# Performance work log

Hardware: AMD Instinct MI355X
Metric: run time of the kernel (lower is better)

Reference implementation:

```python
import jax, jax.numpy as jnp
import numpy as np

H = 51  # hidden size hard-coded in the module

def lstm_cell(x, h, c, W_ih, W_hh, b_ih, b_hh):
    # PyTorch LSTMCell: gates = x @ W_ih^T + b_ih + h @ W_hh^T + b_hh
    g = x @ W_ih.T + h @ W_hh.T + (b_ih + b_hh)  # [B, 4H]
    i, f, gg, o = jnp.split(g, 4, axis=-1)
    c_new = jax.nn.sigmoid(f) * c + jax.nn.sigmoid(i) * jnp.tanh(gg)
    h_new = jax.nn.sigmoid(o) * jnp.tanh(c_new)
    return h_new, c_new

def setup_inputs() -> dict:
    key = jax.random.key(0)
    ks = jax.random.split(key, 12)
    B, T = 2048, 2048
    s1 = 1.0 / np.sqrt(H)
    u = lambda k, shape: jax.random.uniform(k, shape, jnp.float32, -s1, s1)
    return {
        "input": jax.random.normal(ks[0], (B, T), jnp.float32),
        "W_ih1": u(ks[1], (4 * H, 1)),
        "W_hh1": u(ks[2], (4 * H, H)),
        "b_ih1": u(ks[3], (4 * H,)),
        "b_hh1": u(ks[4], (4 * H,)),
        "W_ih2": u(ks[5], (4 * H, H)),
        "W_hh2": u(ks[6], (4 * H, H)),
        "b_ih2": u(ks[7], (4 * H,)),
        "b_hh2": u(ks[8], (4 * H,)),
        "W_lin": u(ks[9], (1, H)),
        "b_lin": u(ks[10], (1,)),
    }

def reference(input, W_ih1, W_hh1, b_ih1, b_hh1, W_ih2, W_hh2, b_ih2, b_hh2, W_lin, b_lin):
    B, T = input.shape
    xs = input.T[:, :, None]  # [T, B, 1]
    h1 = jnp.zeros((B, H), input.dtype)
    c1 = jnp.zeros((B, H), input.dtype)
    h2 = jnp.zeros((B, H), input.dtype)
    c2 = jnp.zeros((B, H), input.dtype)

    def step(carry, x_t):
        h1, c1, h2, c2 = carry
        h1, c1 = lstm_cell(x_t, h1, c1, W_ih1, W_hh1, b_ih1, b_hh1)
        h2, c2 = lstm_cell(h1, h2, c2, W_ih2, W_hh2, b_ih2, b_hh2)
        y = h2 @ W_lin.T + b_lin  # [B, 1]
        return (h1, c1, h2, c2), y[:, 0]

    _, ys = jax.lax.scan(step, (h1, c1, h2, c2), xs)  # ys: [T, B]
    return ys.T  # [B, T]
```

## Files before the change

### kernel.cpp

```cpp
#include <hip/hip_runtime.h>

#define H 51
#define TSEQ 2048
#define BB 16
#define THREADS 1024

typedef _Float16 __attribute__((ext_vector_type(8))) half8;
typedef float    __attribute__((ext_vector_type(4))) float4v;

#define LOG2E    1.44269504f
#define TWOLOG2E 2.88539008f

__device__ __forceinline__ float lstm_ew(float4v a, float& c) {
    float eA = __builtin_amdgcn_exp2f(-a[0]);
    float eB = __builtin_amdgcn_exp2f(a[2]);
    float eF = __builtin_amdgcn_exp2f(-a[1]);
    float pA = eA + 1.0f, pB = eB + 1.0f, pF = eF + 1.0f;
    float dAB = pA * pB;
    float t0  = fmaf(eB, pF, -pF);
    float num = fmaf(c, dAB, t0);
    float r   = __builtin_amdgcn_rcpf(dAB * pF);
    float cn  = num * r;
    c = cn;
    float uD = fminf(cn * TWOLOG2E, 126.0f);
    float eD = __builtin_amdgcn_exp2f(uD);
    float eC = __builtin_amdgcn_exp2f(-a[3]);
    float pD = eD + 1.0f;
    float r2 = __builtin_amdgcn_rcpf(fmaf(eC, pD, pD));
    return fmaf(eD, r2, -r2);
}

__global__ __launch_bounds__(THREADS)
void lstm_w16h_kernel(const float* __restrict__ input,
                      const float* __restrict__ W_ih1, const float* __restrict__ W_hh1,
                      const float* __restrict__ b_ih1, const float* __restrict__ b_hh1,
                      const float* __restrict__ W_ih2, const float* __restrict__ W_hh2,
                      const float* __restrict__ b_ih2, const float* __restrict__ b_hh2,
                      const float* __restrict__ W_lin, const float* __restrict__ b_lin,
                      float* __restrict__ out)
{
    __shared__ half8 hb1[2][2][64];
    __shared__ half8 hb2[2][2][64];
    __shared__ float xss[2][64 * 17];
    __shared__ float ybf[128][17];

    const int tid  = threadIdx.x;
    const int wv   = tid >> 6;
    const int lane = tid & 63;
    const int n    = lane & 15;
    const int qd   = lane >> 4;
    const int b0   = blockIdx.x * BB;
    const float blin = b_lin[0];

    if (tid < 256) {
        half8 z = {0,0,0,0,0,0,0,0};
        (&hb1[0][0][0])[tid] = z;
        (&hb2[0][0][0])[tid] = z;
    }

    if (wv == 15) {
#pragma unroll
        for (int k = 0; k < 16; ++k)
            xss[0][lane * 17 + k] = input[(size_t)(b0 + k) * TSEQ + lane];
    }

    half8 wa1[2];
    half8 wa2[4];
    {
        const int tw1 = (wv < 12) ? wv : ((wv == 13) ? 12 : 13);
        const int tw2 = (wv < 12) ? wv : ((wv == 14) ? 12 : 13);
        {
            const int arow = tw1 * 16 + n;
            const int cell = arow >> 2, gate = arow & 3;
            const int orow = gate * H + cell;
            const float gsc = (gate == 2) ? TWOLOG2E : LOG2E;
            const bool rok = (arow < 4 * H);
#pragma unroll
            for (int s = 0; s < 2; ++s)
#pragma unroll
                for (int j = 0; j < 8; ++j) {
                    int kk = s * 32 + qd * 8 + j;
                    float w = 0.f;
                    if (rok) {
                        if (kk < H)        w = gsc * W_hh1[orow * H + kk];
                        else if (kk == 51) w = gsc * W_ih1[orow];
                    }
                    wa1[s][j] = (_Float16)w;
                }
        }
        {
            const int arow = tw2 * 16 + n;
            const int cell = arow >> 2, gate = arow & 3;
            const int orow = gate * H + cell;
            const float gsc = (gate == 2) ? TWOLOG2E : LOG2E;
            const bool rok = (arow < 4 * H);
#pragma unroll
            for (int s = 0; s < 4; ++s)
#pragma unroll
                for (int j = 0; j < 8; ++j) {
                    int kk = s * 32 + qd * 8 + j;
                    float w = 0.f;
                    if (rok) {
                        if (kk < H)                       w = gsc * W_ih2[orow * H + kk];
                        else if (kk >= 64 && kk < 64 + H) w = gsc * W_hh2[orow * H + (kk - 64)];
                    } else if (arow == 204) {
                        if (kk >= 64 && kk < 64 + H)      w = W_lin[kk - 64];
                    }
                    wa2[s][j] = (_Float16)w;
                }
        }
    }

    const int ewv = (wv == 13 || wv == 14) ? 12 : ((wv < 12) ? wv : 13);
    const int jj  = ewv * 4 + qd;
    float4v bias1v, wih1v, bias2v;
    {
        const bool cok1 = (jj < H) && (wv < 12 || wv == 13);
        const bool cok2 = (jj < H) && (wv < 12 || wv == 14);
#pragma unroll
        for (int r = 0; r < 4; ++r) {
            const float gsc = (r == 2) ? TWOLOG2E : LOG2E;
            const int orow = r * H + jj;
            bias1v[r] = cok1 ? gsc * (b_ih1[orow] + b_hh1[orow]) : 0.f;
            wih1v[r]  = cok1 ? gsc * W_ih1[orow] : 0.f;
            bias2v[r] = cok2 ? gsc * (b_ih2[orow] + b_hh2[orow]) : 0.f;
        }
    }

    float c1 = 0.f, c2 = 0.f;
    const int js = jj >> 5, jq = (jj & 31) >> 3, j7 = jj & 7;

    __syncthreads();

    if (wv < 12 || wv == 13) {
        const float xb = xss[0][n];
        float4v a;
#pragma unroll
        for (int r = 0; r < 4; ++r) a[r] = fmaf(wih1v[r], xb, bias1v[r]);
        float h = lstm_ew(a, c1);
        if (!(wv == 13 && qd == 3))
            ((_Float16*)&hb1[0][js][jq * 16 + n])[j7] = (_Float16)h;
    } else if (wv == 15) {
        if (lane < 16)
            ((_Float16*)&hb1[0][1][32 + lane])[3] = (_Float16)xss[0][17 + lane];
    }
    __syncthreads();

#define STEP(t, P)                                                              \
    {                                                                           \
        if (wv < 12) {                                                          \
               \
            half8 g1[2], g2[2];                                                 \
            g1[0] = hb1[P][0][lane];      g1[1] = hb1[P][1][lane];              \
            float4v a1 = bias1v;                                                \
            a1 = __builtin_amdgcn_mfma_f32_16x16x32_f16(wa1[0], g1[0], a1, 0, 0, 0); \
            a1 = __builtin_amdgcn_mfma_f32_16x16x32_f16(wa1[1], g1[1], a1, 0, 0, 0); \
            float4v a2 = bias2v;                                                \
            a2 = __builtin_amdgcn_mfma_f32_16x16x32_f16(wa2[0], g1[0], a2, 0, 0, 0); \
            a2 = __builtin_amdgcn_mfma_f32_16x16x32_f16(wa2[1], g1[1], a2, 0, 0, 0); \
            __builtin_amdgcn_sched_barrier(0);                                  \
                   \
            g2[0] = hb2[P ^ 1][0][lane];  g2[1] = hb2[P ^ 1][1][lane];          \
            {                                                                   \
                float h = lstm_ew(a1, c1);                                      \
                ((_Float16*)&hb1[P ^ 1][js][jq * 16 + n])[j7] = (_Float16)h;    \
            }                                                                   \
            a2 = __builtin_amdgcn_mfma_f32_16x16x32_f16(wa2[2], g2[0], a2, 0, 0, 0); \
            a2 = __builtin_amdgcn_mfma_f32_16x16x32_f16(wa2[3], g2[1], a2, 0, 0, 0); \
            {                                                                   \
                float h = lstm_ew(a2, c2);                                      \
                ((_Float16*)&hb2[P][js][jq * 16 + n])[j7] = (_Float16)h;        \
            }                                                                   \
        } else if (wv == 12) {                                                  \
               \
            if ((t) > 64 && ((t) & 63) == 1) {                                  \
                const int tb = (t) - 65;                                        \
                const int sb = tb & 127;                                        \
                _Pragma("unroll")                                               \
                for (int r = 0; r < BB; ++r)                                    \
                    out[(size_t)(b0 + r) * TSEQ + tb + lane] = ybf[sb + lane][r]; \
            }                                                                   \
        } else if (wv == 13) {                                                  \
                     \
            half8 g1[2];                                                        \
            g1[0] = hb1[P][0][lane];      g1[1] = hb1[P][1][lane];              \
            float4v a1 = bias1v;                                                \
            a1 = __builtin_amdgcn_mfma_f32_16x16x32_f16(wa1[0], g1[0], a1, 0, 0, 0); \
            a1 = __builtin_amdgcn_mfma_f32_16x16x32_f16(wa1[1], g1[1], a1, 0, 0, 0); \
            float h = lstm_ew(a1, c1);                                          \
            if (qd != 3)                                                        \
                ((_Float16*)&hb1[P ^ 1][js][jq * 16 + n])[j7] = (_Float16)h;    \
        } else if (wv == 14) {                                                  \
               \
            half8 g1[2], g2[2];                                                 \
            g1[0] = hb1[P][0][lane];      g1[1] = hb1[P][1][lane];              \
            float4v a2 = bias2v;                                                \
            a2 = __builtin_amdgcn_mfma_f32_16x16x32_f16(wa2[0], g1[0], a2, 0, 0, 0); \
            a2 = __builtin_amdgcn_mfma_f32_16x16x32_f16(wa2[1], g1[1], a2, 0, 0, 0); \
            __builtin_amdgcn_sched_barrier(0);                                  \
            g2[0] = hb2[P ^ 1][0][lane];  g2[1] = hb2[P ^ 1][1][lane];          \
            a2 = __builtin_amdgcn_mfma_f32_16x16x32_f16(wa2[2], g2[0], a2, 0, 0, 0); \
            a2 = __builtin_amdgcn_mfma_f32_16x16x32_f16(wa2[3], g2[1], a2, 0, 0, 0); \
            float h = lstm_ew(a2, c2);                                          \
            ((_Float16*)&hb2[P][js][jq * 16 + n])[j7] = (_Float16)h;            \
            if (qd == 3) ybf[((t) - 1) & 127][n] = a2[0] + blin;    \
        } else {                                                                \
                \
            const int t2 = (t) + 2;                                             \
            if (lane < 16) {                                                    \
                float xf = xss[(t2 >> 6) & 1][(t2 & 63) * 17 + lane];           \
                ((_Float16*)&hb1[P ^ 1][1][32 + lane])[3] = (_Float16)xf;       \
            }                                                                   \
            if (((t) & 63) == 32 && (t) + 32 < TSEQ) {                          \
                const int cp = ((t) >> 6) & 1;                                  \
                _Pragma("unroll")                                               \
                for (int k = 0; k < 16; ++k)                                    \
                    xss[cp ^ 1][lane * 17 + k] =                                \
                        input[(size_t)(b0 + k) * TSEQ + ((t) + 32) + lane];     \
            }                                                                   \
        }                                                                       \
        __syncthreads();                                                        \
    }

#pragma unroll 1
    for (int t = 0; t < TSEQ; t += 2) {
        STEP(t, 0)
        STEP(t + 1, 1)
    }
#undef STEP

    if (wv == 14) {
        half8 g2a = hb2[1][0][lane], g2b = hb2[1][1][lane];
        float4v yb = (float4v){0.f, 0.f, 0.f, 0.f};
        yb = __builtin_amdgcn_mfma_f32_16x16x32_f16(wa2[2], g2a, yb, 0, 0, 0);
        yb = __builtin_amdgcn_mfma_f32_16x16x32_f16(wa2[3], g2b, yb, 0, 0, 0);
        if (qd == 3) ybf[127][n] = yb[0] + blin;
    }
    __syncthreads();
    if (wv == 12) {
        const int tb = TSEQ - 64;
#pragma unroll
        for (int r = 0; r < BB; ++r)
            out[(size_t)(b0 + r) * TSEQ + tb + lane] = ybf[64 + lane][r];
    }
}

extern "C" void kernel_launch(void* const* d_in, const int* in_sizes, int n_in,
                              void* d_out, int out_size, void* d_ws, size_t ws_size,
                              hipStream_t stream) {
    const float* input = (const float*)d_in[0];
    const float* W_ih1 = (const float*)d_in[1];
    const float* W_hh1 = (const float*)d_in[2];
    const float* b_ih1 = (const float*)d_in[3];
    const float* b_hh1 = (const float*)d_in[4];
    const float* W_ih2 = (const float*)d_in[5];
    const float* W_hh2 = (const float*)d_in[6];
    const float* b_ih2 = (const float*)d_in[7];
    const float* b_hh2 = (const float*)d_in[8];
    const float* W_lin = (const float*)d_in[9];
    const float* b_lin = (const float*)d_in[10];

    lstm_w16h_kernel<<<dim3(2048 / BB), dim3(THREADS), 0, stream>>>(
        input, W_ih1, W_hh1, b_ih1, b_hh1,
        W_ih2, W_hh2, b_ih2, b_hh2, W_lin, b_lin,
        (float*)d_out);
}
```

Measured before the change: 1.209 ms.

## Process two 16-row batch groups per block to interleave independent recurrences

Doubles the batch rows per block to 32, split into two independent 16-row groups. Each wave runs both groups' MFMA and gate chains between the same barriers. This is meant to hide MFMA and transcendental latency through instruction-level parallelism and to amortise per-step barrier cost. In exchange the grid halves to 64 blocks, leaving more CUs idle, and each block does twice the serial work per step.

Result: slower. 1.977 ms (+63.6%).

```diff
diff --git a/kernel.cpp b/kernel.cpp
--- a/kernel.cpp
+++ b/kernel.cpp
@@ -2,7 +2,7 @@
 
 #define H 51
 #define TSEQ 2048
-#define BB 16
+#define BB 32
 #define THREADS 1024
 
 typedef _Float16 __attribute__((ext_vector_type(8))) half8;
@@ -31,18 +31,18 @@
 }
 
 __global__ __launch_bounds__(THREADS)
-void lstm_w16h_kernel(const float* __restrict__ input,
-                      const float* __restrict__ W_ih1, const float* __restrict__ W_hh1,
-                      const float* __restrict__ b_ih1, const float* __restrict__ b_hh1,
-                      const float* __restrict__ W_ih2, const float* __restrict__ W_hh2,
-                      const float* __restrict__ b_ih2, const float* __restrict__ b_hh2,
-                      const float* __restrict__ W_lin, const float* __restrict__ b_lin,
-                      float* __restrict__ out)
+void lstm_w32_kernel(const float* __restrict__ input,
+                     const float* __restrict__ W_ih1, const float* __restrict__ W_hh1,
+                     const float* __restrict__ b_ih1, const float* __restrict__ b_hh1,
+                     const float* __restrict__ W_ih2, const float* __restrict__ W_hh2,
+                     const float* __restrict__ b_ih2, const float* __restrict__ b_hh2,
+                     const float* __restrict__ W_lin, const float* __restrict__ b_lin,
+                     float* __restrict__ out)
 {
-    __shared__ half8 hb1[2][2][64];
-    __shared__ half8 hb2[2][2][64];
-    __shared__ float xss[2][64 * 17];
-    __shared__ float ybf[128][17];
+    __shared__ half8 hb1[2][2][2][64];
+    __shared__ half8 hb2[2][2][2][64];
+    __shared__ float xss[2][2][64 * 17];
+    __shared__ float ybf[2][128][17];
 
     const int tid  = threadIdx.x;
     const int wv   = tid >> 6;
@@ -52,16 +52,17 @@
     const int b0   = blockIdx.x * BB;
     const float blin = b_lin[0];
 
-    if (tid < 256) {
+    if (tid < 512) {
         half8 z = {0,0,0,0,0,0,0,0};
-        (&hb1[0][0][0])[tid] = z;
-        (&hb2[0][0][0])[tid] = z;
+        (&hb1[0][0][0][0])[tid] = z;
+        (&hb2[0][0][0][0])[tid] = z;
     }
 
     if (wv == 15) {
 #pragma unroll
-        for (int k = 0; k < 16; ++k)
-            xss[0][lane * 17 + k] = input[(size_t)(b0 + k) * TSEQ + lane];
+        for (int k = 0; k < 32; ++k)
+            xss[k >> 4][0][lane * 17 + (k & 15)] =
+                input[(size_t)(b0 + k) * TSEQ + lane];
     }
 
     half8 wa1[2];
@@ -127,95 +128,143 @@
         }
     }
 
-    float c1 = 0.f, c2 = 0.f;
+    float c1A = 0.f, c2A = 0.f, c1B = 0.f, c2B = 0.f;
     const int js = jj >> 5, jq = (jj & 31) >> 3, j7 = jj & 7;
 
     __syncthreads();
 
     if (wv < 12 || wv == 13) {
-        const float xb = xss[0][n];
-        float4v a;
-#pragma unroll
-        for (int r = 0; r < 4; ++r) a[r] = fmaf(wih1v[r], xb, bias1v[r]);
-        float h = lstm_ew(a, c1);
-        if (!(wv == 13 && qd == 3))
-            ((_Float16*)&hb1[0][js][jq * 16 + n])[j7] = (_Float16)h;
+        const float xbA = xss[0][0][n];
+        const float xbB = xss[1][0][n];
+        float4v aA, aB;
+#pragma unroll
+        for (int r = 0; r < 4; ++r) {
+            aA[r] = fmaf(wih1v[r], xbA, bias1v[r]);
+            aB[r] = fmaf(wih1v[r], xbB, bias1v[r]);
+        }
+        float hA = lstm_ew(aA, c1A);
+        float hB = lstm_ew(aB, c1B);
+        if (!(wv == 13 && qd == 3)) {
+            ((_Float16*)&hb1[0][0][js][jq * 16 + n])[j7] = (_Float16)hA;
+            ((_Float16*)&hb1[1][0][js][jq * 16 + n])[j7] = (_Float16)hB;
+        }
     } else if (wv == 15) {
-        if (lane < 16)
-            ((_Float16*)&hb1[0][1][32 + lane])[3] = (_Float16)xss[0][17 + lane];
+        if (lane < 32) {
+            int g = lane >> 4, nn = lane & 15;
+            ((_Float16*)&hb1[g][0][1][32 + nn])[3] = (_Float16)xss[g][0][17 + nn];
+        }
     }
     __syncthreads();
 
 #define STEP(t, P)                                                              \
     {                                                                           \
         if (wv < 12) {                                                          \
-               \
-            half8 g1[2], g2[2];                                                 \
-            g1[0] = hb1[P][0][lane];      g1[1] = hb1[P][1][lane];              \
-            float4v a1 = bias1v;                                                \
-            a1 = __builtin_amdgcn_mfma_f32_16x16x32_f16(wa1[0], g1[0], a1, 0, 0, 0); \
-            a1 = __builtin_amdgcn_mfma_f32_16x16x32_f16(wa1[1], g1[1], a1, 0, 0, 0); \
-            float4v a2 = bias2v;                                                \
-            a2 = __builtin_amdgcn_mfma_f32_16x16x32_f16(wa2[0], g1[0], a2, 0, 0, 0); \
-            a2 = __builtin_amdgcn_mfma_f32_16x16x32_f16(wa2[1], g1[1], a2, 0, 0, 0); \
+              \
+            half8 g1A[2], g1B[2], g2A[2], g2B[2];                               \
+            g1A[0] = hb1[0][P][0][lane];  g1A[1] = hb1[0][P][1][lane];          \
+            g1B[0] = hb1[1][P][0][lane];  g1B[1] = hb1[1][P][1][lane];          \
+            float4v a1A = bias1v;                                               \
+            a1A = __builtin_amdgcn_mfma_f32_16x16x32_f16(wa1[0], g1A[0], a1A, 0, 0, 0); \
+            a1A = __builtin_amdgcn_mfma_f32_16x16x32_f16(wa1[1], g1A[1], a1A, 0, 0, 0); \
+            float4v a1B = bias1v;                                               \
+            a1B = __builtin_amdgcn_mfma_f32_16x16x32_f16(wa1[0], g1B[0], a1B, 0, 0, 0); \
+            a1B = __builtin_amdgcn_mfma_f32_16x16x32_f16(wa1[1], g1B[1], a1B, 0, 0, 0); \
+            float4v a2A = bias2v;                                               \
+            a2A = __builtin_amdgcn_mfma_f32_16x16x32_f16(wa2[0], g1A[0], a2A, 0, 0, 0); \
+            a2A = __builtin_amdgcn_mfma_f32_16x16x32_f16(wa2[1], g1A[1], a2A, 0, 0, 0); \
+            float4v a2B = bias2v;                                               \
+            a2B = __builtin_amdgcn_mfma_f32_16x16x32_f16(wa2[0], g1B[0], a2B, 0, 0, 0); \
+            a2B = __builtin_amdgcn_mfma_f32_16x16x32_f16(wa2[1], g1B[1], a2B, 0, 0, 0); \
             __builtin_amdgcn_sched_barrier(0);                                  \
-                   \
-            g2[0] = hb2[P ^ 1][0][lane];  g2[1] = hb2[P ^ 1][1][lane];          \
+              \
+            g2A[0] = hb2[0][P ^ 1][0][lane];  g2A[1] = hb2[0][P ^ 1][1][lane];  \
+            g2B[0] = hb2[1][P ^ 1][0][lane];  g2B[1] = hb2[1][P ^ 1][1][lane];  \
             {                                                                   \
-                float h = lstm_ew(a1, c1);                                      \
-                ((_Float16*)&hb1[P ^ 1][js][jq * 16 + n])[j7] = (_Float16)h;    \
-            }                                                                   \
-            a2 = __builtin_amdgcn_mfma_f32_16x16x32_f16(wa2[2], g2[0], a2, 0, 0, 0); \
-            a2 = __builtin_amdgcn_mfma_f32_16x16x32_f16(wa2[3], g2[1], a2, 0, 0, 0); \
+                float h = lstm_ew(a1A, c1A);                                    \
+                ((_Float16*)&hb1[0][P ^ 1][js][jq * 16 + n])[j7] = (_Float16)h; \
+            }                                                                   \
             {                                                                   \
-                float h = lstm_ew(a2, c2);                                      \
-                ((_Float16*)&hb2[P][js][jq * 16 + n])[j7] = (_Float16)h;        \
+                float h = lstm_ew(a1B, c1B);                                    \
+                ((_Float16*)&hb1[1][P ^ 1][js][jq * 16 + n])[j7] = (_Float16)h; \
+            }                                                                   \
+            a2A = __builtin_amdgcn_mfma_f32_16x16x32_f16(wa2[2], g2A[0], a2A, 0, 0, 0); \
+            a2A = __builtin_amdgcn_mfma_f32_16x16x32_f16(wa2[3], g2A[1], a2A, 0, 0, 0); \
+            a2B = __builtin_amdgcn_mfma_f32_16x16x32_f16(wa2[2], g2B[0], a2B, 0, 0, 0); \
+            a2B = __builtin_amdgcn_mfma_f32_16x16x32_f16(wa2[3], g2B[1], a2B, 0, 0, 0); \
+            {                                                                   \
+                float h = lstm_ew(a2A, c2A);                                    \
+                ((_Float16*)&hb2[0][P][js][jq * 16 + n])[j7] = (_Float16)h;     \
+            }                                                                   \
+            {                                                                   \
+                float h = lstm_ew(a2B, c2B);                                    \
+                ((_Float16*)&hb2[1][P][js][jq * 16 + n])[j7] = (_Float16)h;     \
             }                                                                   \
         } else if (wv == 12) {                                                  \
-               \
+                \
             if ((t) > 64 && ((t) & 63) == 1) {                                  \
                 const int tb = (t) - 65;                                        \
                 const int sb = tb & 127;                                        \
                 _Pragma("unroll")                                               \
                 for (int r = 0; r < BB; ++r)                                    \
-                    out[(size_t)(b0 + r) * TSEQ + tb + lane] = ybf[sb + lane][r]; \
+                    out[(size_t)(b0 + r) * TSEQ + tb + lane] =                  \
+                        ybf[r >> 4][sb + lane][r & 15];                         \
             }                                                                   \
         } else if (wv == 13) {                                                  \
-                     \
-            half8 g1[2];                                                        \
-            g1[0] = hb1[P][0][lane];      g1[1] = hb1[P][1][lane];              \
-            float4v a1 = bias1v;                                                \
-            a1 = __builtin_amdgcn_mfma_f32_16x16x32_f16(wa1[0], g1[0], a1, 0, 0, 0); \
-            a1 = __builtin_amdgcn_mfma_f32_16x16x32_f16(wa1[1], g1[1], a1, 0, 0, 0); \
-            float h = lstm_ew(a1, c1);                                          \
-            if (qd != 3)                                                        \
-                ((_Float16*)&hb1[P ^ 1][js][jq * 16 + n])[j7] = (_Float16)h;    \
+                    \
+            half8 g1A[2], g1B[2];                                               \
+            g1A[0] = hb1[0][P][0][lane];  g1A[1] = hb1[0][P][1][lane];          \
+            g1B[0] = hb1[1][P][0][lane];  g1B[1] = hb1[1][P][1][lane];          \
+            float4v a1A = bias1v;                                               \
+            a1A = __builtin_amdgcn_mfma_f32_16x16x32_f16(wa1[0], g1A[0], a1A, 0, 0, 0); \
+            a1A = __builtin_amdgcn_mfma_f32_16x16x32_f16(wa1[1], g1A[1], a1A, 0, 0, 0); \
+            float4v a1B = bias1v;                                               \
+            a1B = __builtin_amdgcn_mfma_f32_16x16x32_f16(wa1[0], g1B[0], a1B, 0, 0, 0); \
+            a1B = __builtin_amdgcn_mfma_f32_16x16x32_f16(wa1[1], g1B[1], a1B, 0, 0, 0); \
+            float hA = lstm_ew(a1A, c1A);                                       \
+            float hB = lstm_ew(a1B, c1B);                                       \
+            if (qd != 3) {                                                      \
+                ((_Float16*)&hb1[0][P ^ 1][js][jq * 16 + n])[j7] = (_Float16)hA; \
+                ((_Float16*)&hb1[1][P ^ 1][js][jq * 16 + n])[j7] = (_Float16)hB; \
+            }                                                                   \
         } else if (wv == 14) {                                                  \
-               \
-            half8 g1[2], g2[2];                                                 \
-            g1[0] = hb1[P][0][lane];      g1[1] = hb1[P][1][lane];              \
-            float4v a2 = bias2v;                                                \
-            a2 = __builtin_amdgcn_mfma_f32_16x16x32_f16(wa2[0], g1[0], a2, 0, 0, 0); \
-            a2 = __builtin_amdgcn_mfma_f32_16x16x32_f16(wa2[1], g1[1], a2, 0, 0, 0); \
+                   \
+            half8 g1A[2], g1B[2], g2A[2], g2B[2];                               \
+            g1A[0] = hb1[0][P][0][lane];  g1A[1] = hb1[0][P][1][lane];          \
+            g1B[0] = hb1[1][P][0][lane];  g1B[1] = hb1[1][P][1][lane];          \
+            float4v a2A = bias2v;                                               \
+            a2A = __builtin_amdgcn_mfma_f32_16x16x32_f16(wa2[0], g1A[0], a2A, 0, 0, 0); \
+            a2A = __builtin_amdgcn_mfma_f32_16x16x32_f16(wa2[1], g1A[1], a2A, 0, 0, 0); \
+            float4v a2B = bias2v;                                               \
+            a2B = __builtin_amdgcn_mfma_f32_16x16x32_f16(wa2[0], g1B[0], a2B, 0, 0, 0); \
+            a2B = __builtin_amdgcn_mfma_f32_16x16x32_f16(wa2[1], g1B[1], a2B, 0, 0, 0); \
             __builtin_amdgcn_sched_barrier(0);                                  \
-            g2[0] = hb2[P ^ 1][0][lane];  g2[1] = hb2[P ^ 1][1][lane];          \
-            a2 = __builtin_amdgcn_mfma_f32_16x16x32_f16(wa2[2], g2[0], a2, 0, 0, 0); \
-            a2 = __builtin_amdgcn_mfma_f32_16x16x32_f16(wa2[3], g2[1], a2, 0, 0, 0); \
-            float h = lstm_ew(a2, c2);                                          \
-            ((_Float16*)&hb2[P][js][jq * 16 + n])[j7] = (_Float16)h;            \
-            if (qd == 3) ybf[((t) - 1) & 127][n] = a2[0] + blin;    \
+            g2A[0] = hb2[0][P ^ 1][0][lane];  g2A[1] = hb2[0][P ^ 1][1][lane];  \
+            g2B[0] = hb2[1][P ^ 1][0][lane];  g2B[1] = hb2[1][P ^ 1][1][lane];  \
+            a2A = __builtin_amdgcn_mfma_f32_16x16x32_f16(wa2[2], g2A[0], a2A, 0, 0, 0); \
+            a2A = __builtin_amdgcn_mfma_f32_16x16x32_f16(wa2[3], g2A[1], a2A, 0, 0, 0); \
+            a2B = __builtin_amdgcn_mfma_f32_16x16x32_f16(wa2[2], g2B[0], a2B, 0, 0, 0); \
+            a2B = __builtin_amdgcn_mfma_f32_16x16x32_f16(wa2[3], g2B[1], a2B, 0, 0, 0); \
+            float hA = lstm_ew(a2A, c2A);                                       \
+            float hB = lstm_ew(a2B, c2B);                                       \
+            ((_Float16*)&hb2[0][P][js][jq * 16 + n])[j7] = (_Float16)hA;        \
+            ((_Float16*)&hb2[1][P][js][jq * 16 + n])[j7] = (_Float16)hB;        \
+            if (qd == 3) {                                                      \
+                ybf[0][((t) - 1) & 127][n] = a2A[0] + blin;                     \
+                ybf[1][((t) - 1) & 127][n] = a2B[0] + blin;                     \
+            }                                                                   \
         } else {                                                                \
-                \
+                      \
             const int t2 = (t) + 2;                                             \
-            if (lane < 16) {                                                    \
-                float xf = xss[(t2 >> 6) & 1][(t2 & 63) * 17 + lane];           \
-                ((_Float16*)&hb1[P ^ 1][1][32 + lane])[3] = (_Float16)xf;       \
+            if (lane < 32) {                                                    \
+                int g = lane >> 4, nn = lane & 15;                              \
+                float xf = xss[g][(t2 >> 6) & 1][(t2 & 63) * 17 + nn];          \
+                ((_Float16*)&hb1[g][P ^ 1][1][32 + nn])[3] = (_Float16)xf;      \
             }                                                                   \
             if (((t) & 63) == 32 && (t) + 32 < TSEQ) {                          \
                 const int cp = ((t) >> 6) & 1;                                  \
                 _Pragma("unroll")                                               \
-                for (int k = 0; k < 16; ++k)                                    \
-                    xss[cp ^ 1][lane * 17 + k] =                                \
+                for (int k = 0; k < 32; ++k)                                    \
+                    xss[k >> 4][cp ^ 1][lane * 17 + (k & 15)] =                 \
                         input[(size_t)(b0 + k) * TSEQ + ((t) + 32) + lane];     \
             }                                                                   \
         }                                                                       \
@@ -230,18 +279,21 @@
 #undef STEP
 
     if (wv == 14) {
-        half8 g2a = hb2[1][0][lane], g2b = hb2[1][1][lane];
-        float4v yb = (float4v){0.f, 0.f, 0.f, 0.f};
-        yb = __builtin_amdgcn_mfma_f32_16x16x32_f16(wa2[2], g2a, yb, 0, 0, 0);
-        yb = __builtin_amdgcn_mfma_f32_16x16x32_f16(wa2[3], g2b, yb, 0, 0, 0);
-        if (qd == 3) ybf[127][n] = yb[0] + blin;
+#pragma unroll
+        for (int g = 0; g < 2; ++g) {
+            half8 g2a = hb2[g][1][0][lane], g2b = hb2[g][1][1][lane];
+            float4v yb = (float4v){0.f, 0.f, 0.f, 0.f};
+            yb = __builtin_amdgcn_mfma_f32_16x16x32_f16(wa2[2], g2a, yb, 0, 0, 0);
+            yb = __builtin_amdgcn_mfma_f32_16x16x32_f16(wa2[3], g2b, yb, 0, 0, 0);
+            if (qd == 3) ybf[g][127][n] = yb[0] + blin;
+        }
     }
     __syncthreads();
     if (wv == 12) {
         const int tb = TSEQ - 64;
 #pragma unroll
         for (int r = 0; r < BB; ++r)
-            out[(size_t)(b0 + r) * TSEQ + tb + lane] = ybf[64 + lane][r];
+            out[(size_t)(b0 + r) * TSEQ + tb + lane] = ybf[r >> 4][64 + lane][r & 15];
     }
 }
 
@@ -260,7 +312,7 @@
     const float* W_lin = (const float*)d_in[9];
     const float* b_lin = (const float*)d_in[10];
 
-    lstm_w16h_kernel<<<dim3(2048 / BB), dim3(THREADS), 0, stream>>>(
+    lstm_w32_kernel<<<dim3(2048 / BB), dim3(THREADS), 0, stream>>>(
         input, W_ih1, W_hh1, b_ih1, b_hh1,
         W_ih2, W_hh2, b_ih2, b_hh2, W_lin, b_lin,
         (float*)d_out);
```
